# Kernel tuning notes

Measured on AMD Instinct MI355X. Metric: run time of the kernel, lower is better.

## Reference

```python
import jax, jax.numpy as jnp
import numpy as np

EMBED = 256; NH = 8; NP = 32; STRIDE = 4; FFN = 1024
NUM_IMG = 4; H = 160; W = 160; NOBJ = 2048
HD = EMBED // NH
LN_EPS = 1e-5


def setup_inputs():
    key = jax.random.key(0)
    ks = jax.random.split(key, 16)
    inp = {}
    inp["query"] = jax.random.normal(ks[0], (NOBJ, NH, 1, HD), jnp.float32)
    inp["obj_emb"] = jax.random.normal(ks[1], (NOBJ, EMBED), jnp.float32)
    inp["key_feat"] = jax.random.normal(ks[2], (NUM_IMG, EMBED, H, W), jnp.float32)
    inp["value"] = jax.random.normal(ks[3], (NUM_IMG, EMBED, H, W), jnp.float32)
    ys, xs = jnp.meshgrid(jnp.arange(H, dtype=jnp.float32), jnp.arange(W, dtype=jnp.float32), indexing="ij")
    x2d = jnp.stack([(xs + 0.5) * STRIDE, (ys + 0.5) * STRIDE], axis=0)  # (2,H,W) pixel coords
    inp["img_dense_x2d"] = jnp.broadcast_to(x2d[None], (NUM_IMG, 2, H, W)).astype(jnp.float32)
    inp["img_dense_x2d_mask"] = (jax.random.uniform(ks[4], (NUM_IMG, 1, H, W)) > 0.1).astype(jnp.float32)
    inp["obj_xy_point"] = jax.random.uniform(ks[5], (NOBJ, 2)) * jnp.array([W * STRIDE, H * STRIDE], jnp.float32)
    inp["strides"] = 2.0 ** jax.random.randint(ks[6], (NOBJ,), 2, 5).astype(jnp.float32)  # {4,8,16}
    inp["obj_img_ind"] = jax.random.randint(ks[7], (NOBJ,), 0, NUM_IMG, dtype=jnp.int32)
    s = 1.0 / np.sqrt(EMBED)
    inp["w_off"] = jax.random.uniform(ks[8], (EMBED, NH * NP * 2), minval=-s, maxval=s) * 2.5
    inp["b_off"] = jnp.zeros((NH * NP * 2,), jnp.float32)
    inp["w_out"] = jax.random.uniform(ks[9], (EMBED, EMBED), minval=-s, maxval=s)
    inp["b_out"] = jnp.zeros((EMBED,), jnp.float32)
    inp["ln1_g"] = jnp.ones((EMBED,), jnp.float32)
    inp["ln1_b"] = jnp.zeros((EMBED,), jnp.float32)
    inp["w1"] = jax.random.uniform(ks[10], (EMBED, FFN), minval=-s, maxval=s)
    inp["b1"] = jnp.zeros((FFN,), jnp.float32)
    sf = 1.0 / np.sqrt(FFN)
    inp["w2"] = jax.random.uniform(ks[11], (FFN, EMBED), minval=-sf, maxval=sf)
    inp["b2"] = jnp.zeros((EMBED,), jnp.float32)
    inp["ln2_g"] = jnp.ones((EMBED,), jnp.float32)
    inp["ln2_b"] = jnp.zeros((EMBED,), jnp.float32)
    return inp


def _unnorm(g, size):
    # align_corners=False: pixel index = ((g+1)*size - 1) / 2
    return ((g + 1.0) * size - 1.0) * 0.5


def _bilinear(gather, gx, gy, w_size, h_size, zeros_pad):
    """Bilinear sample. gather(y,x) -> (..., C). border or zeros padding."""
    ix = _unnorm(gx, w_size)
    iy = _unnorm(gy, h_size)
    x0f = jnp.floor(ix); y0f = jnp.floor(iy)
    wx1 = ix - x0f; wy1 = iy - y0f
    x0 = x0f.astype(jnp.int32); y0 = y0f.astype(jnp.int32)
    out = None
    for dx, dy, wgt in ((0, 0, (1 - wx1) * (1 - wy1)), (1, 0, wx1 * (1 - wy1)),
                        (0, 1, (1 - wx1) * wy1), (1, 1, wx1 * wy1)):
        xi = x0 + dx; yi = y0 + dy
        xc = jnp.clip(xi, 0, w_size - 1); yc = jnp.clip(yi, 0, h_size - 1)
        if zeros_pad:
            valid = (xi >= 0) & (xi < w_size) & (yi >= 0) & (yi < h_size)
            wgt = wgt * valid.astype(wgt.dtype)
        term = gather(yc, xc) * wgt[..., None]
        out = term if out is None else out + term
    return out


def _ln(x, g, b):
    m = x.mean(-1, keepdims=True)
    v = jnp.mean(jnp.square(x - m), axis=-1, keepdims=True)
    return (x - m) * jax.lax.rsqrt(v + LN_EPS) * g + b


def _forward(query, obj_emb, key_feat, value, img_dense_x2d, img_dense_x2d_mask,
             obj_xy_point, strides, obj_img_ind,
             w_off, b_off, w_out, b_out, ln1_g, ln1_b, w1, b1, w2, b2, ln2_g, ln2_b):
    N = query.shape[0]
    offsets = (obj_emb @ w_off + b_off).reshape(N, NH, NP, 2)
    loc = obj_xy_point[:, None, None] + offsets * strides[:, None, None, None]  # (N,NH,NP,2)
    gx = loc[..., 0] * (2.0 / (W * STRIDE)) - 1.0
    gy = loc[..., 1] * (2.0 / (H * STRIDE)) - 1.0
    # z grid coordinate lands exactly on slice obj_img_ind (zero depth fraction),
    # so 3D trilinear grid_sample reduces to 2D bilinear on the selected image.
    img = obj_img_ind[:, None, None]          # (N,1,1)
    head = jnp.arange(NH)[None, :, None]      # (1,NH,1)
    key_r = key_feat.reshape(NUM_IMG, NH, HD, H, W)
    val_r = value.reshape(NUM_IMG, NH, HD, H, W)
    k_s = _bilinear(lambda y, x: key_r[img, head, :, y, x], gx, gy, W, H, False)   # (N,NH,NP,HD)
    v_s = _bilinear(lambda y, x: val_r[img, head, :, y, x], gx, gy, W, H, False)   # (N,NH,NP,HD)
    x2d_s = _bilinear(lambda y, x: img_dense_x2d[img, :, y, x], gx, gy, W, H, False)       # (N,NH,NP,2)
    mask_s = _bilinear(lambda y, x: img_dense_x2d_mask[img, :, y, x], gx, gy, W, H, True)  # (N,NH,NP,1)
    q = query[:, :, 0]  # (N,NH,HD)
    a = jnp.einsum('nhd,nhpd->nhp', q, k_s) / np.sqrt(HD)
    a_sm = jax.nn.softmax(a, axis=-1) * mask_s[..., 0]
    out = jnp.einsum('nhpd,nhp->nhd', v_s, a_sm).reshape(N, EMBED)
    out = out @ w_out + b_out + obj_emb
    out = _ln(out, ln1_g, ln1_b)
    out = out + (jax.nn.relu(out @ w1 + b1) @ w2 + b2)
    out = _ln(out, ln2_g, ln2_b)
    v_samples = jnp.swapaxes(v_s, -1, -2)      # (N,NH,HD,NP)
    a_samples = a[:, :, None, :]               # (N,NH,1,NP)
    mask_samples = jnp.swapaxes(mask_s, -1, -2)  # (N,NH,1,NP)
    x2d_samples = jnp.swapaxes(x2d_s, -1, -2)    # (N,NH,2,NP)
    return (out, v_samples, a_samples, mask_samples, x2d_samples)


def reference(query, obj_emb, key_feat, value, img_dense_x2d, img_dense_x2d_mask,
              obj_xy_point, strides, obj_img_ind,
              w_off, b_off, w_out, b_out, ln1_g, ln1_b, w1, b1, w2, b2, ln2_g, ln2_b):
    return _forward(query, obj_emb, key_feat, value, img_dense_x2d, img_dense_x2d_mask,
                    obj_xy_point, strides, obj_img_ind,
                    w_off, b_off, w_out, b_out, ln1_g, ln1_b, w1, b1, w2, b2, ln2_g, ln2_b)
```

## Files before the change

kernel.cpp:

```cpp
#include <hip/hip_runtime.h>
#include <hip/hip_fp16.h>
#include <math.h>

#define NOBJ  2048
#define EMBED 256
#define NHD   8
#define NPT   32
#define HD    32
#define NUMIMG 4
#define HH    160
#define WW    160
#define FFN   1024
#define PLANE (HH*WW)
#define LN_EPS 1e-5f

typedef _Float16 f16x8 __attribute__((ext_vector_type(8)));
typedef float f32x4 __attribute__((ext_vector_type(4)));

__global__ __launch_bounds__(256) void k_offsets(
    const float* __restrict__ obj_emb, const float* __restrict__ w_off,
    const float* __restrict__ b_off, const float* __restrict__ obj_xy,
    const float* __restrict__ strides,
    float* __restrict__ cx, float* __restrict__ cy) {
  const int G = 8;
  __shared__ float s_emb[G][EMBED];
  const int t = threadIdx.x;
  const int n0 = blockIdx.x * G;
  #pragma unroll
  for (int g = 0; g < G; ++g) s_emb[g][t] = obj_emb[(n0 + g) * EMBED + t];
  __syncthreads();

  float ax[G], ay[G];
  #pragma unroll
  for (int g = 0; g < G; ++g) { ax[g] = 0.f; ay[g] = 0.f; }

  const float2* wp = (const float2*)w_off;
  for (int e = 0; e < EMBED; ++e) {
    float2 w = wp[e * 256 + t];
    #pragma unroll
    for (int g = 0; g < G; ++g) {
      float a = s_emb[g][e];
      ax[g] = fmaf(a, w.x, ax[g]);
      ay[g] = fmaf(a, w.y, ay[g]);
    }
  }
  const float bx = b_off[2 * t], by = b_off[2 * t + 1];
  #pragma unroll
  for (int g = 0; g < G; ++g) {
    const int n = n0 + g;
    const float st = strides[n];
    const float lx = obj_xy[2 * n]     + (ax[g] + bx) * st;
    const float ly = obj_xy[2 * n + 1] + (ay[g] + by) * st;
    const float gx = lx * (2.0f / (WW * 4)) - 1.0f;
    const float gy = ly * (2.0f / (HH * 4)) - 1.0f;
    const float ix = ((gx + 1.0f) * WW - 1.0f) * 0.5f;
    const float iy = ((gy + 1.0f) * HH - 1.0f) * 0.5f;
    cx[n * 256 + t] = ix;
    cy[n * 256 + t] = iy;
  }
}

__global__ __launch_bounds__(512) void k_relayout(
    const float* __restrict__ key_feat, const float* __restrict__ value,
    __half* __restrict__ kvh, int img_base) {
  __shared__ __half s[320][144];
  const int t = threadIdx.x;
  const int Y   = blockIdx.x;
  const int hp  = blockIdx.y;
  const int img = img_base + blockIdx.z;
  const int pl  = t >> 2;
  const int q   = t & 3;

  const int sub  = pl & 31;
  const int grp  = pl >> 5;
  const int head = hp * 2 + (grp >> 1);
  const int ch   = head * 32 + sub;
  const float* src = (grp & 1) ? value : key_feat;
  const float* sp  = src + ((size_t)img * 256 + ch) * PLANE
                   + (size_t)Y * 320 + q * 80;
  const int pxq = q * 80;

  #pragma unroll
  for (int i0 = 0; i0 < 20; i0 += 10) {
    float4 r[10];
    #pragma unroll
    for (int i = 0; i < 10; ++i) r[i] = *(const float4*)(sp + (i0 + i) * 4);
    #pragma unroll
    for (int i = 0; i < 10; ++i) {
      const int px = pxq + (i0 + i) * 4;
      s[px + 0][pl] = __float2half(r[i].x);
      s[px + 1][pl] = __float2half(r[i].y);
      s[px + 2][pl] = __float2half(r[i].z);
      s[px + 3][pl] = __float2half(r[i].w);
    }
  }
  __syncthreads();

  const size_t rec = (size_t)img * PLANE + (size_t)Y * 320;
  #pragma unroll
  for (int it = 0; it < 10; ++it) {
    const int flat = it * 512 + t;
    const int px = flat >> 4, j = flat & 15;
    const int4 v = *(const int4*)&s[px][j * 8];
    *(int4*)(kvh + (rec + px) * 512 + hp * 128 + j * 8) = v;
  }
}

__device__ __forceinline__ void acc8(int4 r, float w, float* acc) {
  const __half2* hp = (const __half2*)&r;
  #pragma unroll
  for (int i = 0; i < 4; ++i) {
    const float2 f = __half22float2(hp[i]);
    acc[2 * i]     = fmaf(w, f.x, acc[2 * i]);
    acc[2 * i + 1] = fmaf(w, f.y, acc[2 * i + 1]);
  }
}

__global__ __launch_bounds__(256) void k_sample_hwc(
    const float* __restrict__ query, const __half* __restrict__ kvh,
    const float* __restrict__ x2d, const float* __restrict__ x2d_mask,
    const int* __restrict__ obj_img,
    const float* __restrict__ cx, const float* __restrict__ cy,
    float* __restrict__ o_vs, float* __restrict__ o_as,
    float* __restrict__ o_ms, float* __restrict__ o_x2,
    _Float16* __restrict__ attn_h) {
  __shared__ float s_q[256];
  __shared__ float s_v[NHD * NPT * 33];
  __shared__ float s_asm[256];

  const int n = blockIdx.x;
  const int t = threadIdx.x;
  const int h = t >> 5, p = t & 31;

  s_q[t] = query[n * 256 + t];
  const int img = obj_img[n];
  const float ix = cx[n * 256 + t];
  const float iy = cy[n * 256 + t];

  const float x0f = floorf(ix), y0f = floorf(iy);
  const float wx1 = ix - x0f, wy1 = iy - y0f;
  const int x0 = (int)x0f, y0 = (int)y0f;
  const int x1 = x0 + 1, y1 = y0 + 1;
  const int x0c = min(max(x0, 0), WW - 1), x1c = min(max(x1, 0), WW - 1);
  const int y0c = min(max(y0, 0), HH - 1), y1c = min(max(y1, 0), HH - 1);
  const float w00 = (1.f - wx1) * (1.f - wy1);
  const float w10 = wx1 * (1.f - wy1);
  const float w01 = (1.f - wx1) * wy1;
  const float w11 = wx1 * wy1;
  const int o00 = y0c * WW + x0c, o10 = y0c * WW + x1c;
  const int o01 = y1c * WW + x0c, o11 = y1c * WW + x1c;

  const size_t pb = (size_t)img * PLANE;
  const int4* base = (const int4*)kvh;
  const long b0 = ((long)(pb + o00)) * 64 + h * 8;
  const long b1 = ((long)(pb + o10)) * 64 + h * 8;
  const long b2 = ((long)(pb + o01)) * 64 + h * 8;
  const long b3 = ((long)(pb + o11)) * 64 + h * 8;
  __syncthreads();

  float a_acc = 0.f;
  float* svrow = &s_v[(h * NPT + p) * 33];
  float* vout = o_vs + (size_t)(n * NHD + h) * (HD * NPT) + p;
  #pragma unroll
  for (int ch = 0; ch < 4; ++ch) {
    const int4 k0 = base[b0 + ch],     k1 = base[b1 + ch];
    const int4 k2 = base[b2 + ch],     k3 = base[b3 + ch];
    const int4 v0 = base[b0 + 4 + ch], v1 = base[b1 + 4 + ch];
    const int4 v2 = base[b2 + 4 + ch], v3 = base[b3 + 4 + ch];
    float kc[8] = {0, 0, 0, 0, 0, 0, 0, 0};
    float vc[8] = {0, 0, 0, 0, 0, 0, 0, 0};
    acc8(k0, w00, kc); acc8(k1, w10, kc); acc8(k2, w01, kc); acc8(k3, w11, kc);
    acc8(v0, w00, vc); acc8(v1, w10, vc); acc8(v2, w01, vc); acc8(v3, w11, vc);
    #pragma unroll
    for (int j = 0; j < 8; ++j) {
      const int c = ch * 8 + j;
      a_acc = fmaf(s_q[h * HD + c], kc[j], a_acc);
      svrow[c] = vc[j];
      vout[c * NPT] = vc[j];
    }
  }

  const float a = a_acc * 0.17677669529663687f;
  o_as[n * 256 + t] = a;

  const float* xb0 = x2d + (size_t)img * 2 * PLANE;
  const float* xb1 = xb0 + PLANE;
  const float x2v0 = w00 * xb0[o00] + w10 * xb0[o10] + w01 * xb0[o01] + w11 * xb0[o11];
  const float x2v1 = w00 * xb1[o00] + w10 * xb1[o10] + w01 * xb1[o01] + w11 * xb1[o11];
  o_x2[(size_t)n * 512 + h * 64 + p]      = x2v0;
  o_x2[(size_t)n * 512 + h * 64 + 32 + p] = x2v1;

  const float* mb = x2d_mask + (size_t)img * PLANE;
  const float m00 = (x0 >= 0 && x0 < WW && y0 >= 0 && y0 < HH) ? w00 : 0.f;
  const float m10 = (x1 >= 0 && x1 < WW && y0 >= 0 && y0 < HH) ? w10 : 0.f;
  const float m01 = (x0 >= 0 && x0 < WW && y1 >= 0 && y1 < HH) ? w01 : 0.f;
  const float m11 = (x1 >= 0 && x1 < WW && y1 >= 0 && y1 < HH) ? w11 : 0.f;
  const float m = m00 * mb[o00] + m10 * mb[o10] + m01 * mb[o01] + m11 * mb[o11];
  o_ms[n * 256 + t] = m;

  float mx = a;
  #pragma unroll
  for (int o = 16; o >= 1; o >>= 1) mx = fmaxf(mx, __shfl_xor(mx, o, 32));
  const float ev = expf(a - mx);
  float s = ev;
  #pragma unroll
  for (int o = 16; o >= 1; o >>= 1) s += __shfl_xor(s, o, 32);
  s_asm[t] = ev / s * m;
  __syncthreads();

  const int d = p;
  float o = 0.f;
  const float* svh = &s_v[h * NPT * 33];
  const float* amh = &s_asm[h * NPT];
  #pragma unroll
  for (int pp = 0; pp < NPT; ++pp) o = fmaf(amh[pp], svh[pp * 33 + d], o);
  attn_h[n * 256 + t] = (_Float16)o;
}

__global__ __launch_bounds__(256) void k_cvtw_all(
    const float* __restrict__ w_out, const float* __restrict__ w1,
    const float* __restrict__ w2, _Float16* __restrict__ woT,
    _Float16* __restrict__ w1T, _Float16* __restrict__ w2T) {
  __shared__ float s[32][33];
  const int id = blockIdx.x;
  const float* w; _Float16* wT; int K, N, kt, nt;
  if (id < 64)       { w = w_out; wT = woT; K = 256;  N = 256;
                       kt = id & 7;  nt = id >> 3; }
  else if (id < 320) { const int r = id - 64;  w = w1; wT = w1T;
                       K = 256;  N = 1024; kt = r & 7;  nt = r >> 3; }
  else               { const int r = id - 320; w = w2; wT = w2T;
                       K = 1024; N = 256;  kt = r & 31; nt = r >> 5; }
  const int t = threadIdx.x;
  const int k0 = kt * 32, n0 = nt * 32;
  const int nl = t & 31, kg = t >> 5;
  #pragma unroll
  for (int i = 0; i < 4; ++i) {
    const int k = kg * 4 + i;
    s[k][nl] = w[(size_t)(k0 + k) * N + n0 + nl];
  }
  __syncthreads();
  const int kl = t & 31, ng = t >> 5;
  #pragma unroll
  for (int i = 0; i < 4; ++i) {
    const int n = ng * 4 + i;
    wT[(size_t)(n0 + n) * K + k0 + kl] = (_Float16)s[kl][n];
  }
}


__global__ __launch_bounds__(256) void k_gemm_a(
    const _Float16* __restrict__ Ah, const _Float16* __restrict__ BT,
    float* __restrict__ C) {
  const int t = threadIdx.x;
  const int wv = t >> 6, lane = t & 63;
  const int r16 = lane & 15, quad = lane >> 4;
  const int m_base = blockIdx.x * 64 + wv * 16;
  const int n_base = blockIdx.y * 32;
  const _Float16* ap  = Ah + (size_t)(m_base + r16) * 256 + quad * 8;
  const _Float16* bp0 = BT + (size_t)(n_base + r16) * 256 + quad * 8;
  const _Float16* bp1 = bp0 + 16 * 256;
  f32x4 acc0 = {0.f, 0.f, 0.f, 0.f}, acc1 = {0.f, 0.f, 0.f, 0.f};
  #pragma unroll 4
  for (int kc = 0; kc < 256; kc += 32) {
    f16x8 a  = *(const f16x8*)(ap + kc);
    f16x8 b0 = *(const f16x8*)(bp0 + kc);
    f16x8 b1 = *(const f16x8*)(bp1 + kc);
    acc0 = __builtin_amdgcn_mfma_f32_16x16x32_f16(a, b0, acc0, 0, 0, 0);
    acc1 = __builtin_amdgcn_mfma_f32_16x16x32_f16(a, b1, acc1, 0, 0, 0);
  }
  float* cp = C + (size_t)(m_base + quad * 4) * 256 + n_base + r16;
  #pragma unroll
  for (int r = 0; r < 4; ++r) {
    cp[(size_t)r * 256]      = acc0[r];
    cp[(size_t)r * 256 + 16] = acc1[r];
  }
}

__global__ __launch_bounds__(256) void k_gemm_b(
    const _Float16* __restrict__ Ah, const _Float16* __restrict__ BT,
    const float* __restrict__ bias, _Float16* __restrict__ Fh) {
  const int t = threadIdx.x;
  const int wv = t >> 6, lane = t & 63;
  const int r16 = lane & 15, quad = lane >> 4;
  const int m_base = blockIdx.x * 64 + wv * 16;
  const int n_base = blockIdx.y * 32;
  const _Float16* ap  = Ah + (size_t)(m_base + r16) * 256 + quad * 8;
  const _Float16* bp0 = BT + (size_t)(n_base + r16) * 256 + quad * 8;
  const _Float16* bp1 = bp0 + 16 * 256;
  f32x4 acc0 = {0.f, 0.f, 0.f, 0.f}, acc1 = {0.f, 0.f, 0.f, 0.f};
  #pragma unroll 4
  for (int kc = 0; kc < 256; kc += 32) {
    f16x8 a  = *(const f16x8*)(ap + kc);
    f16x8 b0 = *(const f16x8*)(bp0 + kc);
    f16x8 b1 = *(const f16x8*)(bp1 + kc);
    acc0 = __builtin_amdgcn_mfma_f32_16x16x32_f16(a, b0, acc0, 0, 0, 0);
    acc1 = __builtin_amdgcn_mfma_f32_16x16x32_f16(a, b1, acc1, 0, 0, 0);
  }
  const float bb0 = bias[n_base + r16];
  const float bb1 = bias[n_base + 16 + r16];
  _Float16* fp = Fh + (size_t)(m_base + quad * 4) * 1024 + n_base + r16;
  #pragma unroll
  for (int r = 0; r < 4; ++r) {
    fp[(size_t)r * 1024]      = (_Float16)fmaxf(acc0[r] + bb0, 0.f);
    fp[(size_t)r * 1024 + 16] = (_Float16)fmaxf(acc1[r] + bb1, 0.f);
  }
}

__global__ __launch_bounds__(256) void k_gemm_c(
    const _Float16* __restrict__ Ah, const _Float16* __restrict__ BT,
    float* __restrict__ C) {
  const int t = threadIdx.x;
  const int wv = t >> 6, lane = t & 63;
  const int r16 = lane & 15, quad = lane >> 4;
  const int m_base = blockIdx.x * 64 + wv * 16;
  const int n_base = blockIdx.y * 32;
  const _Float16* ap  = Ah + (size_t)(m_base + r16) * 1024 + quad * 8;
  const _Float16* bp0 = BT + (size_t)(n_base + r16) * 1024 + quad * 8;
  const _Float16* bp1 = bp0 + 16 * 1024;
  f32x4 acc0 = {0.f, 0.f, 0.f, 0.f}, acc1 = {0.f, 0.f, 0.f, 0.f};
  #pragma unroll 4
  for (int kc = 0; kc < 1024; kc += 32) {
    f16x8 a  = *(const f16x8*)(ap + kc);
    f16x8 b0 = *(const f16x8*)(bp0 + kc);
    f16x8 b1 = *(const f16x8*)(bp1 + kc);
    acc0 = __builtin_amdgcn_mfma_f32_16x16x32_f16(a, b0, acc0, 0, 0, 0);
    acc1 = __builtin_amdgcn_mfma_f32_16x16x32_f16(a, b1, acc1, 0, 0, 0);
  }
  float* cp = C + (size_t)(m_base + quad * 4) * 256 + n_base + r16;
  #pragma unroll
  for (int r = 0; r < 4; ++r) {
    cp[(size_t)r * 256]      = acc0[r];
    cp[(size_t)r * 256 + 16] = acc1[r];
  }
}

__global__ __launch_bounds__(256) void k_ln1(
    const float* __restrict__ Y1, const float* __restrict__ b_out,
    const float* __restrict__ obj_emb, const float* __restrict__ g,
    const float* __restrict__ b, float* __restrict__ U,
    _Float16* __restrict__ Uh) {
  __shared__ float s_y[8][EMBED + 8];
  const int t = threadIdx.x;
  const int m0 = blockIdx.x * 8;
  const float bo = b_out[t];
  #pragma unroll
  for (int r = 0; r < 8; ++r)
    s_y[r][t] = Y1[(size_t)(m0 + r) * EMBED + t] + bo
                + obj_emb[(size_t)(m0 + r) * EMBED + t];
  __syncthreads();
  const int wv = t >> 6, ln = t & 63;
  #pragma unroll
  for (int k = 0; k < 2; ++k) {
    const int rr = wv * 2 + k;
    const float v0 = s_y[rr][ln], v1 = s_y[rr][ln + 64];
    const float v2 = s_y[rr][ln + 128], v3 = s_y[rr][ln + 192];
    float sum = v0 + v1 + v2 + v3;
    #pragma unroll
    for (int o = 32; o >= 1; o >>= 1) sum += __shfl_xor(sum, o);
    const float mean = sum * (1.0f / EMBED);
    const float d0 = v0 - mean, d1 = v1 - mean, d2 = v2 - mean, d3 = v3 - mean;
    float ss = d0 * d0 + d1 * d1 + d2 * d2 + d3 * d3;
    #pragma unroll
    for (int o = 32; o >= 1; o >>= 1) ss += __shfl_xor(ss, o);
    const float rstd = rsqrtf(ss * (1.0f / EMBED) + LN_EPS);
    const size_t base = (size_t)(m0 + rr) * EMBED;
    const float o0 = d0 * rstd * g[ln]       + b[ln];
    const float o1 = d1 * rstd * g[ln + 64]  + b[ln + 64];
    const float o2 = d2 * rstd * g[ln + 128] + b[ln + 128];
    const float o3 = d3 * rstd * g[ln + 192] + b[ln + 192];
    U[base + ln] = o0;         Uh[base + ln] = (_Float16)o0;
    U[base + ln + 64] = o1;    Uh[base + ln + 64] = (_Float16)o1;
    U[base + ln + 128] = o2;   Uh[base + ln + 128] = (_Float16)o2;
    U[base + ln + 192] = o3;   Uh[base + ln + 192] = (_Float16)o3;
  }
}

__global__ __launch_bounds__(256) void k_ln2(
    const float* __restrict__ Y2, const float* __restrict__ b2,
    const float* __restrict__ U, const float* __restrict__ g,
    const float* __restrict__ b, float* __restrict__ out) {
  __shared__ float s_y[8][EMBED + 8];
  const int t = threadIdx.x;
  const int m0 = blockIdx.x * 8;
  const float bb = b2[t];
  #pragma unroll
  for (int r = 0; r < 8; ++r)
    s_y[r][t] = Y2[(size_t)(m0 + r) * EMBED + t] + bb
                + U[(size_t)(m0 + r) * EMBED + t];
  __syncthreads();
  const int wv = t >> 6, ln = t & 63;
  #pragma unroll
  for (int k = 0; k < 2; ++k) {
    const int rr = wv * 2 + k;
    const float v0 = s_y[rr][ln], v1 = s_y[rr][ln + 64];
    const float v2 = s_y[rr][ln + 128], v3 = s_y[rr][ln + 192];
    float sum = v0 + v1 + v2 + v3;
    #pragma unroll
    for (int o = 32; o >= 1; o >>= 1) sum += __shfl_xor(sum, o);
    const float mean = sum * (1.0f / EMBED);
    const float d0 = v0 - mean, d1 = v1 - mean, d2 = v2 - mean, d3 = v3 - mean;
    float ss = d0 * d0 + d1 * d1 + d2 * d2 + d3 * d3;
    #pragma unroll
    for (int o = 32; o >= 1; o >>= 1) ss += __shfl_xor(ss, o);
    const float rstd = rsqrtf(ss * (1.0f / EMBED) + LN_EPS);
    const size_t base = (size_t)(m0 + rr) * EMBED;
    out[base + ln]       = d0 * rstd * g[ln]       + b[ln];
    out[base + ln + 64]  = d1 * rstd * g[ln + 64]  + b[ln + 64];
    out[base + ln + 128] = d2 * rstd * g[ln + 128] + b[ln + 128];
    out[base + ln + 192] = d3 * rstd * g[ln + 192] + b[ln + 192];
  }
}

extern "C" void kernel_launch(void* const* d_in, const int* in_sizes, int n_in,
                              void* d_out, int out_size, void* d_ws, size_t ws_size,
                              hipStream_t stream) {
  const float* query    = (const float*)d_in[0];
  const float* obj_emb  = (const float*)d_in[1];
  const float* key_feat = (const float*)d_in[2];
  const float* value    = (const float*)d_in[3];
  const float* x2d      = (const float*)d_in[4];
  const float* x2d_mask = (const float*)d_in[5];
  const float* obj_xy   = (const float*)d_in[6];
  const float* strides  = (const float*)d_in[7];
  const int*   obj_img  = (const int*)d_in[8];
  const float* w_off    = (const float*)d_in[9];
  const float* b_off    = (const float*)d_in[10];
  const float* w_out    = (const float*)d_in[11];
  const float* b_out    = (const float*)d_in[12];
  const float* ln1_g    = (const float*)d_in[13];
  const float* ln1_b    = (const float*)d_in[14];
  const float* w1       = (const float*)d_in[15];
  const float* b1       = (const float*)d_in[16];
  const float* w2       = (const float*)d_in[17];
  const float* b2       = (const float*)d_in[18];
  const float* ln2_g    = (const float*)d_in[19];
  const float* ln2_b    = (const float*)d_in[20];

  float* out = (float*)d_out;
  float* o_out = out;
  float* o_vs  = out + 524288;
  float* o_as  = out + 524288 + 16777216;
  float* o_ms  = out + 524288 + 16777216 + 524288;
  float* o_x2  = out + 524288 + 16777216 + 1048576;

  char* wsb = (char*)d_ws;
  __half*    kvh    = (__half*)wsb;
  char* B = wsb + 104857600;
  float*     cx     = (float*)(B);
  float*     Y1     = (float*)(B);
  float*     cy     = (float*)(B + 2097152);
  float*     Y2     = (float*)(B + 2097152);
  float*     U      = (float*)(B + 4194304);
  _Float16*  Fh     = (_Float16*)(B + 6291456);
  _Float16*  attn_h = (_Float16*)(B + 10485760);
  _Float16*  Uh     = (_Float16*)(B + 11534336);
  _Float16*  woT    = (_Float16*)(B + 12582912);
  _Float16*  w1T    = (_Float16*)(B + 12582912 + 131072);
  _Float16*  w2T    = (_Float16*)(B + 12582912 + 131072 + 524288);

  k_offsets<<<NOBJ / 8, 256, 0, stream>>>(obj_emb, w_off, b_off, obj_xy,
                                          strides, cx, cy);
  k_relayout<<<dim3(80, 4, 2), 512, 0, stream>>>(key_feat, value, kvh, 0);
  k_relayout<<<dim3(80, 4, 2), 512, 0, stream>>>(key_feat, value, kvh, 2);
  k_cvtw_all<<<576, 256, 0, stream>>>(w_out, w1, w2, woT, w1T, w2T);
  k_sample_hwc<<<NOBJ, 256, 0, stream>>>(query, kvh, x2d, x2d_mask, obj_img,
                                         cx, cy, o_vs, o_as, o_ms, o_x2,
                                         attn_h);
  k_gemm_a<<<dim3(32, 8), 256, 0, stream>>>(attn_h, woT, Y1);
  k_ln1<<<NOBJ / 8, 256, 0, stream>>>(Y1, b_out, obj_emb, ln1_g, ln1_b, U, Uh);
  k_gemm_b<<<dim3(32, 32), 256, 0, stream>>>(Uh, w1T, b1, Fh);
  k_gemm_c<<<dim3(32, 8), 256, 0, stream>>>(Fh, w2T, Y2);
  k_ln2<<<NOBJ / 8, 256, 0, stream>>>(Y2, b2, U, ln2_g, ln2_b, o_out);
}
```

Before: 447.4 us.

## Fuse post-attention GEMMs and layernorms into one tail kernel; merge prep kernels

Replaces the five tail kernels (out-proj GEMM, LN1, FFN up GEMM, FFN down GEMM, LN2) with a single 512-thread kernel that processes 16 rows per block and keeps intermediates in shared memory. This removes global round-trips for Y1, U, Uh, Fh and Y2, and cuts launch overhead. The offset computation and weight conversion are merged into one launch, and the sampling kernel now stages V in fp16 shared memory to shrink LDS use. Trade-offs: the tail now runs only 128 blocks, which limits parallelism, and LN variance is computed as E[x²]−mean², which is less numerically precise.

```diff
diff --git a/kernel.cpp b/kernel.cpp
--- a/kernel.cpp
+++ b/kernel.cpp
@@ -17,46 +17,71 @@
 typedef _Float16 f16x8 __attribute__((ext_vector_type(8)));
 typedef float f32x4 __attribute__((ext_vector_type(4)));
 
-__global__ __launch_bounds__(256) void k_offsets(
+__global__ __launch_bounds__(256) void k_prep(
     const float* __restrict__ obj_emb, const float* __restrict__ w_off,
     const float* __restrict__ b_off, const float* __restrict__ obj_xy,
     const float* __restrict__ strides,
-    float* __restrict__ cx, float* __restrict__ cy) {
-  const int G = 8;
-  __shared__ float s_emb[G][EMBED];
+    float* __restrict__ cx, float* __restrict__ cy,
+    const float* __restrict__ w_out, const float* __restrict__ w1,
+    const float* __restrict__ w2, _Float16* __restrict__ woT,
+    _Float16* __restrict__ w1T, _Float16* __restrict__ w2T) {
+  __shared__ float s_emb[8][EMBED];
+  __shared__ float s_t[32][33];
   const int t = threadIdx.x;
-  const int n0 = blockIdx.x * G;
-  #pragma unroll
-  for (int g = 0; g < G; ++g) s_emb[g][t] = obj_emb[(n0 + g) * EMBED + t];
-  __syncthreads();
-
-  float ax[G], ay[G];
-  #pragma unroll
-  for (int g = 0; g < G; ++g) { ax[g] = 0.f; ay[g] = 0.f; }
-
-  const float2* wp = (const float2*)w_off;
-  for (int e = 0; e < EMBED; ++e) {
-    float2 w = wp[e * 256 + t];
+  if (blockIdx.x < 256) {
+    const int G = 8;
+    const int n0 = blockIdx.x * G;
+    #pragma unroll
+    for (int g = 0; g < G; ++g) s_emb[g][t] = obj_emb[(n0 + g) * EMBED + t];
+    __syncthreads();
+    float ax[G], ay[G];
+    #pragma unroll
+    for (int g = 0; g < G; ++g) { ax[g] = 0.f; ay[g] = 0.f; }
+    const float2* wp = (const float2*)w_off;
+    for (int e = 0; e < EMBED; ++e) {
+      float2 w = wp[e * 256 + t];
+      #pragma unroll
+      for (int g = 0; g < G; ++g) {
+        float a = s_emb[g][e];
+        ax[g] = fmaf(a, w.x, ax[g]);
+        ay[g] = fmaf(a, w.y, ay[g]);
+      }
+    }
+    const float bx = b_off[2 * t], by = b_off[2 * t + 1];
     #pragma unroll
     for (int g = 0; g < G; ++g) {
-      float a = s_emb[g][e];
-      ax[g] = fmaf(a, w.x, ax[g]);
-      ay[g] = fmaf(a, w.y, ay[g]);
-    }
-  }
-  const float bx = b_off[2 * t], by = b_off[2 * t + 1];
-  #pragma unroll
-  for (int g = 0; g < G; ++g) {
-    const int n = n0 + g;
-    const float st = strides[n];
-    const float lx = obj_xy[2 * n]     + (ax[g] + bx) * st;
-    const float ly = obj_xy[2 * n + 1] + (ay[g] + by) * st;
-    const float gx = lx * (2.0f / (WW * 4)) - 1.0f;
-    const float gy = ly * (2.0f / (HH * 4)) - 1.0f;
-    const float ix = ((gx + 1.0f) * WW - 1.0f) * 0.5f;
-    const float iy = ((gy + 1.0f) * HH - 1.0f) * 0.5f;
-    cx[n * 256 + t] = ix;
-    cy[n * 256 + t] = iy;
+      const int n = n0 + g;
+      const float st = strides[n];
+      const float lx = obj_xy[2 * n]     + (ax[g] + bx) * st;
+      const float ly = obj_xy[2 * n + 1] + (ay[g] + by) * st;
+      const float gx = lx * (2.0f / (WW * 4)) - 1.0f;
+      const float gy = ly * (2.0f / (HH * 4)) - 1.0f;
+      cx[n * 256 + t] = ((gx + 1.0f) * WW - 1.0f) * 0.5f;
+      cy[n * 256 + t] = ((gy + 1.0f) * HH - 1.0f) * 0.5f;
+    }
+  } else {
+    const int id = blockIdx.x - 256;
+    const float* w; _Float16* wT; int K, N, kt, nt;
+    if (id < 64)       { w = w_out; wT = woT; K = 256;  N = 256;
+                         kt = id & 7;  nt = id >> 3; }
+    else if (id < 320) { const int r = id - 64;  w = w1; wT = w1T;
+                         K = 256;  N = 1024; kt = r & 7;  nt = r >> 3; }
+    else               { const int r = id - 320; w = w2; wT = w2T;
+                         K = 1024; N = 256;  kt = r & 31; nt = r >> 5; }
+    const int k0 = kt * 32, n0 = nt * 32;
+    const int nl = t & 31, kg = t >> 5;
+    #pragma unroll
+    for (int i = 0; i < 4; ++i) {
+      const int k = kg * 4 + i;
+      s_t[k][nl] = w[(size_t)(k0 + k) * N + n0 + nl];
+    }
+    __syncthreads();
+    const int kl = t & 31, ng = t >> 5;
+    #pragma unroll
+    for (int i = 0; i < 4; ++i) {
+      const int n = ng * 4 + i;
+      wT[(size_t)(n0 + n) * K + k0 + kl] = (_Float16)s_t[kl][n];
+    }
   }
 }
 
@@ -125,7 +150,7 @@
     float* __restrict__ o_ms, float* __restrict__ o_x2,
     _Float16* __restrict__ attn_h) {
   __shared__ float s_q[256];
-  __shared__ float s_v[NHD * NPT * 33];
+  __shared__ _Float16 s_v[NHD * NPT * 34];
   __shared__ float s_asm[256];
 
   const int n = blockIdx.x;
@@ -159,7 +184,7 @@
   __syncthreads();
 
   float a_acc = 0.f;
-  float* svrow = &s_v[(h * NPT + p) * 33];
+  _Float16* svrow = &s_v[(h * NPT + p) * 34];
   float* vout = o_vs + (size_t)(n * NHD + h) * (HD * NPT) + p;
   #pragma unroll
   for (int ch = 0; ch < 4; ++ch) {
@@ -175,7 +200,7 @@
     for (int j = 0; j < 8; ++j) {
       const int c = ch * 8 + j;
       a_acc = fmaf(s_q[h * HD + c], kc[j], a_acc);
-      svrow[c] = vc[j];
+      svrow[c] = (_Float16)vc[j];
       vout[c * NPT] = vc[j];
     }
   }
@@ -210,204 +235,159 @@
 
   const int d = p;
   float o = 0.f;
-  const float* svh = &s_v[h * NPT * 33];
+  const _Float16* svh = &s_v[h * NPT * 34];
   const float* amh = &s_asm[h * NPT];
   #pragma unroll
-  for (int pp = 0; pp < NPT; ++pp) o = fmaf(amh[pp], svh[pp * 33 + d], o);
+  for (int pp = 0; pp < NPT; ++pp)
+    o = fmaf(amh[pp], (float)svh[pp * 34 + d], o);
   attn_h[n * 256 + t] = (_Float16)o;
 }
 
-__global__ __launch_bounds__(256) void k_cvtw_all(
-    const float* __restrict__ w_out, const float* __restrict__ w1,
-    const float* __restrict__ w2, _Float16* __restrict__ woT,
-    _Float16* __restrict__ w1T, _Float16* __restrict__ w2T) {
-  __shared__ float s[32][33];
-  const int id = blockIdx.x;
-  const float* w; _Float16* wT; int K, N, kt, nt;
-  if (id < 64)       { w = w_out; wT = woT; K = 256;  N = 256;
-                       kt = id & 7;  nt = id >> 3; }
-  else if (id < 320) { const int r = id - 64;  w = w1; wT = w1T;
-                       K = 256;  N = 1024; kt = r & 7;  nt = r >> 3; }
-  else               { const int r = id - 320; w = w2; wT = w2T;
-                       K = 1024; N = 256;  kt = r & 31; nt = r >> 5; }
-  const int t = threadIdx.x;
-  const int k0 = kt * 32, n0 = nt * 32;
-  const int nl = t & 31, kg = t >> 5;
-  #pragma unroll
-  for (int i = 0; i < 4; ++i) {
-    const int k = kg * 4 + i;
-    s[k][nl] = w[(size_t)(k0 + k) * N + n0 + nl];
-  }
-  __syncthreads();
-  const int kl = t & 31, ng = t >> 5;
-  #pragma unroll
-  for (int i = 0; i < 4; ++i) {
-    const int n = ng * 4 + i;
-    wT[(size_t)(n0 + n) * K + k0 + kl] = (_Float16)s[kl][n];
-  }
-}
-
-
-__global__ __launch_bounds__(256) void k_gemm_a(
-    const _Float16* __restrict__ Ah, const _Float16* __restrict__ BT,
-    float* __restrict__ C) {
+__global__ __launch_bounds__(512) void k_tail(
+    const _Float16* __restrict__ attn_h, const _Float16* __restrict__ woT,
+    const _Float16* __restrict__ w1T, const _Float16* __restrict__ w2T,
+    const float* __restrict__ b_out, const float* __restrict__ obj_emb,
+    const float* __restrict__ g1, const float* __restrict__ bb1,
+    const float* __restrict__ b1, const float* __restrict__ b2,
+    const float* __restrict__ g2, const float* __restrict__ bb2,
+    float* __restrict__ out) {
+  __shared__ _Float16 sUh[16][264];
+  __shared__ float    sU [16][264];
+  __shared__ _Float16 sF [16][1032];
+  __shared__ float    sP[8][16];
+  __shared__ float    sQ[8][16];
   const int t = threadIdx.x;
   const int wv = t >> 6, lane = t & 63;
   const int r16 = lane & 15, quad = lane >> 4;
-  const int m_base = blockIdx.x * 64 + wv * 16;
-  const int n_base = blockIdx.y * 32;
-  const _Float16* ap  = Ah + (size_t)(m_base + r16) * 256 + quad * 8;
-  const _Float16* bp0 = BT + (size_t)(n_base + r16) * 256 + quad * 8;
-  const _Float16* bp1 = bp0 + 16 * 256;
-  f32x4 acc0 = {0.f, 0.f, 0.f, 0.f}, acc1 = {0.f, 0.f, 0.f, 0.f};
-  #pragma unroll 4
-  for (int kc = 0; kc < 256; kc += 32) {
-    f16x8 a  = *(const f16x8*)(ap + kc);
-    f16x8 b0 = *(const f16x8*)(bp0 + kc);
-    f16x8 b1 = *(const f16x8*)(bp1 + kc);
-    acc0 = __builtin_amdgcn_mfma_f32_16x16x32_f16(a, b0, acc0, 0, 0, 0);
-    acc1 = __builtin_amdgcn_mfma_f32_16x16x32_f16(a, b1, acc1, 0, 0, 0);
-  }
-  float* cp = C + (size_t)(m_base + quad * 4) * 256 + n_base + r16;
-  #pragma unroll
-  for (int r = 0; r < 4; ++r) {
-    cp[(size_t)r * 256]      = acc0[r];
-    cp[(size_t)r * 256 + 16] = acc1[r];
-  }
-}
-
-__global__ __launch_bounds__(256) void k_gemm_b(
-    const _Float16* __restrict__ Ah, const _Float16* __restrict__ BT,
-    const float* __restrict__ bias, _Float16* __restrict__ Fh) {
-  const int t = threadIdx.x;
-  const int wv = t >> 6, lane = t & 63;
-  const int r16 = lane & 15, quad = lane >> 4;
-  const int m_base = blockIdx.x * 64 + wv * 16;
-  const int n_base = blockIdx.y * 32;
-  const _Float16* ap  = Ah + (size_t)(m_base + r16) * 256 + quad * 8;
-  const _Float16* bp0 = BT + (size_t)(n_base + r16) * 256 + quad * 8;
-  const _Float16* bp1 = bp0 + 16 * 256;
-  f32x4 acc0 = {0.f, 0.f, 0.f, 0.f}, acc1 = {0.f, 0.f, 0.f, 0.f};
-  #pragma unroll 4
-  for (int kc = 0; kc < 256; kc += 32) {
-    f16x8 a  = *(const f16x8*)(ap + kc);
-    f16x8 b0 = *(const f16x8*)(bp0 + kc);
-    f16x8 b1 = *(const f16x8*)(bp1 + kc);
-    acc0 = __builtin_amdgcn_mfma_f32_16x16x32_f16(a, b0, acc0, 0, 0, 0);
-    acc1 = __builtin_amdgcn_mfma_f32_16x16x32_f16(a, b1, acc1, 0, 0, 0);
-  }
-  const float bb0 = bias[n_base + r16];
-  const float bb1 = bias[n_base + 16 + r16];
-  _Float16* fp = Fh + (size_t)(m_base + quad * 4) * 1024 + n_base + r16;
-  #pragma unroll
-  for (int r = 0; r < 4; ++r) {
-    fp[(size_t)r * 1024]      = (_Float16)fmaxf(acc0[r] + bb0, 0.f);
-    fp[(size_t)r * 1024 + 16] = (_Float16)fmaxf(acc1[r] + bb1, 0.f);
-  }
-}
-
-__global__ __launch_bounds__(256) void k_gemm_c(
-    const _Float16* __restrict__ Ah, const _Float16* __restrict__ BT,
-    float* __restrict__ C) {
-  const int t = threadIdx.x;
-  const int wv = t >> 6, lane = t & 63;
-  const int r16 = lane & 15, quad = lane >> 4;
-  const int m_base = blockIdx.x * 64 + wv * 16;
-  const int n_base = blockIdx.y * 32;
-  const _Float16* ap  = Ah + (size_t)(m_base + r16) * 1024 + quad * 8;
-  const _Float16* bp0 = BT + (size_t)(n_base + r16) * 1024 + quad * 8;
-  const _Float16* bp1 = bp0 + 16 * 1024;
-  f32x4 acc0 = {0.f, 0.f, 0.f, 0.f}, acc1 = {0.f, 0.f, 0.f, 0.f};
-  #pragma unroll 4
-  for (int kc = 0; kc < 1024; kc += 32) {
-    f16x8 a  = *(const f16x8*)(ap + kc);
-    f16x8 b0 = *(const f16x8*)(bp0 + kc);
-    f16x8 b1 = *(const f16x8*)(bp1 + kc);
-    acc0 = __builtin_amdgcn_mfma_f32_16x16x32_f16(a, b0, acc0, 0, 0, 0);
-    acc1 = __builtin_amdgcn_mfma_f32_16x16x32_f16(a, b1, acc1, 0, 0, 0);
-  }
-  float* cp = C + (size_t)(m_base + quad * 4) * 256 + n_base + r16;
-  #pragma unroll
-  for (int r = 0; r < 4; ++r) {
-    cp[(size_t)r * 256]      = acc0[r];
-    cp[(size_t)r * 256 + 16] = acc1[r];
-  }
-}
-
-__global__ __launch_bounds__(256) void k_ln1(
-    const float* __restrict__ Y1, const float* __restrict__ b_out,
-    const float* __restrict__ obj_emb, const float* __restrict__ g,
-    const float* __restrict__ b, float* __restrict__ U,
-    _Float16* __restrict__ Uh) {
-  __shared__ float s_y[8][EMBED + 8];
-  const int t = threadIdx.x;
-  const int m0 = blockIdx.x * 8;
-  const float bo = b_out[t];
-  #pragma unroll
-  for (int r = 0; r < 8; ++r)
-    s_y[r][t] = Y1[(size_t)(m0 + r) * EMBED + t] + bo
-                + obj_emb[(size_t)(m0 + r) * EMBED + t];
+  const int m0 = blockIdx.x * 16;
+
+  {
+    const int c0 = wv * 32;
+    const _Float16* ap  = attn_h + (size_t)(m0 + r16) * 256 + quad * 8;
+    const _Float16* bp0 = woT + (size_t)(c0 + r16) * 256 + quad * 8;
+    const _Float16* bp1 = bp0 + 16 * 256;
+    f32x4 acc0 = {0.f,0.f,0.f,0.f}, acc1 = {0.f,0.f,0.f,0.f};
+    #pragma unroll
+    for (int kc = 0; kc < 256; kc += 32) {
+      f16x8 a  = *(const f16x8*)(ap + kc);
+      f16x8 b0 = *(const f16x8*)(bp0 + kc);
+      f16x8 b1f = *(const f16x8*)(bp1 + kc);
+      acc0 = __builtin_amdgcn_mfma_f32_16x16x32_f16(a, b0, acc0, 0, 0, 0);
+      acc1 = __builtin_amdgcn_mfma_f32_16x16x32_f16(a, b1f, acc1, 0, 0, 0);
+    }
+    const int col0 = c0 + r16, col1 = c0 + 16 + r16;
+    const float bo0 = b_out[col0], bo1 = b_out[col1];
+    float v0[4], v1[4];
+    #pragma unroll
+    for (int r = 0; r < 4; ++r) {
+      const size_t row = (size_t)(m0 + quad * 4 + r) * 256;
+      v0[r] = acc0[r] + bo0 + obj_emb[row + col0];
+      v1[r] = acc1[r] + bo1 + obj_emb[row + col1];
+    }
+    #pragma unroll
+    for (int r = 0; r < 4; ++r) {
+      float s = v0[r] + v1[r];
+      float q = v0[r] * v0[r] + v1[r] * v1[r];
+      #pragma unroll
+      for (int m = 1; m < 16; m <<= 1) {
+        s += __shfl_xor(s, m);
+        q += __shfl_xor(q, m);
+      }
+      if (r16 == 0) { sP[wv][quad * 4 + r] = s; sQ[wv][quad * 4 + r] = q; }
+    }
+    __syncthreads();
+    const float g0 = g1[col0], be0 = bb1[col0];
+    const float g1v = g1[col1], be1 = bb1[col1];
+    #pragma unroll
+    for (int r = 0; r < 4; ++r) {
+      const int rr = quad * 4 + r;
+      float S = 0.f, Q = 0.f;
+      #pragma unroll
+      for (int w = 0; w < 8; ++w) { S += sP[w][rr]; Q += sQ[w][rr]; }
+      const float mean = S * (1.0f / EMBED);
+      const float var  = Q * (1.0f / EMBED) - mean * mean;
+      const float rstd = rsqrtf(var + LN_EPS);
+      const float u0 = (v0[r] - mean) * rstd * g0 + be0;
+      const float u1 = (v1[r] - mean) * rstd * g1v + be1;
+      sU[rr][col0] = u0;  sUh[rr][col0] = (_Float16)u0;
+      sU[rr][col1] = u1;  sUh[rr][col1] = (_Float16)u1;
+    }
+  }
   __syncthreads();
-  const int wv = t >> 6, ln = t & 63;
-  #pragma unroll
-  for (int k = 0; k < 2; ++k) {
-    const int rr = wv * 2 + k;
-    const float v0 = s_y[rr][ln], v1 = s_y[rr][ln + 64];
-    const float v2 = s_y[rr][ln + 128], v3 = s_y[rr][ln + 192];
-    float sum = v0 + v1 + v2 + v3;
-    #pragma unroll
-    for (int o = 32; o >= 1; o >>= 1) sum += __shfl_xor(sum, o);
-    const float mean = sum * (1.0f / EMBED);
-    const float d0 = v0 - mean, d1 = v1 - mean, d2 = v2 - mean, d3 = v3 - mean;
-    float ss = d0 * d0 + d1 * d1 + d2 * d2 + d3 * d3;
-    #pragma unroll
-    for (int o = 32; o >= 1; o >>= 1) ss += __shfl_xor(ss, o);
-    const float rstd = rsqrtf(ss * (1.0f / EMBED) + LN_EPS);
-    const size_t base = (size_t)(m0 + rr) * EMBED;
-    const float o0 = d0 * rstd * g[ln]       + b[ln];
-    const float o1 = d1 * rstd * g[ln + 64]  + b[ln + 64];
-    const float o2 = d2 * rstd * g[ln + 128] + b[ln + 128];
-    const float o3 = d3 * rstd * g[ln + 192] + b[ln + 192];
-    U[base + ln] = o0;         Uh[base + ln] = (_Float16)o0;
-    U[base + ln + 64] = o1;    Uh[base + ln + 64] = (_Float16)o1;
-    U[base + ln + 128] = o2;   Uh[base + ln + 128] = (_Float16)o2;
-    U[base + ln + 192] = o3;   Uh[base + ln + 192] = (_Float16)o3;
-  }
-}
-
-__global__ __launch_bounds__(256) void k_ln2(
-    const float* __restrict__ Y2, const float* __restrict__ b2,
-    const float* __restrict__ U, const float* __restrict__ g,
-    const float* __restrict__ b, float* __restrict__ out) {
-  __shared__ float s_y[8][EMBED + 8];
-  const int t = threadIdx.x;
-  const int m0 = blockIdx.x * 8;
-  const float bb = b2[t];
-  #pragma unroll
-  for (int r = 0; r < 8; ++r)
-    s_y[r][t] = Y2[(size_t)(m0 + r) * EMBED + t] + bb
-                + U[(size_t)(m0 + r) * EMBED + t];
+
+  {
+    const int c0 = wv * 128;
+    f32x4 acc[8];
+    #pragma unroll
+    for (int i = 0; i < 8; ++i) acc[i] = (f32x4){0.f,0.f,0.f,0.f};
+    for (int kc = 0; kc < 256; kc += 32) {
+      f16x8 a = *(const f16x8*)&sUh[r16][quad * 8 + kc];
+      #pragma unroll
+      for (int nt = 0; nt < 8; ++nt) {
+        f16x8 b = *(const f16x8*)(w1T + (size_t)(c0 + nt * 16 + r16) * 256
+                                  + quad * 8 + kc);
+        acc[nt] = __builtin_amdgcn_mfma_f32_16x16x32_f16(a, b, acc[nt], 0, 0, 0);
+      }
+    }
+    #pragma unroll
+    for (int nt = 0; nt < 8; ++nt) {
+      const int col = c0 + nt * 16 + r16;
+      const float bb = b1[col];
+      #pragma unroll
+      for (int r = 0; r < 4; ++r)
+        sF[quad * 4 + r][col] = (_Float16)fmaxf(acc[nt][r] + bb, 0.f);
+    }
+  }
   __syncthreads();
-  const int wv = t >> 6, ln = t & 63;
-  #pragma unroll
-  for (int k = 0; k < 2; ++k) {
-    const int rr = wv * 2 + k;
-    const float v0 = s_y[rr][ln], v1 = s_y[rr][ln + 64];
-    const float v2 = s_y[rr][ln + 128], v3 = s_y[rr][ln + 192];
-    float sum = v0 + v1 + v2 + v3;
-    #pragma unroll
-    for (int o = 32; o >= 1; o >>= 1) sum += __shfl_xor(sum, o);
-    const float mean = sum * (1.0f / EMBED);
-    const float d0 = v0 - mean, d1 = v1 - mean, d2 = v2 - mean, d3 = v3 - mean;
-    float ss = d0 * d0 + d1 * d1 + d2 * d2 + d3 * d3;
-    #pragma unroll
-    for (int o = 32; o >= 1; o >>= 1) ss += __shfl_xor(ss, o);
-    const float rstd = rsqrtf(ss * (1.0f / EMBED) + LN_EPS);
-    const size_t base = (size_t)(m0 + rr) * EMBED;
-    out[base + ln]       = d0 * rstd * g[ln]       + b[ln];
-    out[base + ln + 64]  = d1 * rstd * g[ln + 64]  + b[ln + 64];
-    out[base + ln + 128] = d2 * rstd * g[ln + 128] + b[ln + 128];
-    out[base + ln + 192] = d3 * rstd * g[ln + 192] + b[ln + 192];
+
+  {
+    const int c0 = wv * 32;
+    const _Float16* bp0 = w2T + (size_t)(c0 + r16) * 1024 + quad * 8;
+    const _Float16* bp1 = bp0 + 16 * 1024;
+    f32x4 acc0 = {0.f,0.f,0.f,0.f}, acc1 = {0.f,0.f,0.f,0.f};
+    for (int kc = 0; kc < 1024; kc += 32) {
+      f16x8 a  = *(const f16x8*)&sF[r16][quad * 8 + kc];
+      f16x8 b0 = *(const f16x8*)(bp0 + kc);
+      f16x8 b1f = *(const f16x8*)(bp1 + kc);
+      acc0 = __builtin_amdgcn_mfma_f32_16x16x32_f16(a, b0, acc0, 0, 0, 0);
+      acc1 = __builtin_amdgcn_mfma_f32_16x16x32_f16(a, b1f, acc1, 0, 0, 0);
+    }
+    const int col0 = c0 + r16, col1 = c0 + 16 + r16;
+    const float bo0 = b2[col0], bo1 = b2[col1];
+    float v0[4], v1[4];
+    #pragma unroll
+    for (int r = 0; r < 4; ++r) {
+      const int rr = quad * 4 + r;
+      v0[r] = acc0[r] + bo0 + sU[rr][col0];
+      v1[r] = acc1[r] + bo1 + sU[rr][col1];
+    }
+    #pragma unroll
+    for (int r = 0; r < 4; ++r) {
+      float s = v0[r] + v1[r];
+      float q = v0[r] * v0[r] + v1[r] * v1[r];
+      #pragma unroll
+      for (int m = 1; m < 16; m <<= 1) {
+        s += __shfl_xor(s, m);
+        q += __shfl_xor(q, m);
+      }
+      if (r16 == 0) { sP[wv][quad * 4 + r] = s; sQ[wv][quad * 4 + r] = q; }
+    }
+    __syncthreads();
+    const float g0 = g2[col0], be0 = bb2[col0];
+    const float g1v = g2[col1], be1 = bb2[col1];
+    #pragma unroll
+    for (int r = 0; r < 4; ++r) {
+      const int rr = quad * 4 + r;
+      float S = 0.f, Q = 0.f;
+      #pragma unroll
+      for (int w = 0; w < 8; ++w) { S += sP[w][rr]; Q += sQ[w][rr]; }
+      const float mean = S * (1.0f / EMBED);
+      const float var  = Q * (1.0f / EMBED) - mean * mean;
+      const float rstd = rsqrtf(var + LN_EPS);
+      const size_t row = (size_t)(m0 + rr) * 256;
+      out[row + col0] = (v0[r] - mean) * rstd * g0 + be0;
+      out[row + col1] = (v1[r] - mean) * rstd * g1v + be1;
+    }
   }
 }
 
@@ -447,28 +427,20 @@
   __half*    kvh    = (__half*)wsb;
   char* B = wsb + 104857600;
   float*     cx     = (float*)(B);
-  float*     Y1     = (float*)(B);
   float*     cy     = (float*)(B + 2097152);
-  float*     Y2     = (float*)(B + 2097152);
-  float*     U      = (float*)(B + 4194304);
-  _Float16*  Fh     = (_Float16*)(B + 6291456);
-  _Float16*  attn_h = (_Float16*)(B + 10485760);
-  _Float16*  Uh     = (_Float16*)(B + 11534336);
-  _Float16*  woT    = (_Float16*)(B + 12582912);
-  _Float16*  w1T    = (_Float16*)(B + 12582912 + 131072);
-  _Float16*  w2T    = (_Float16*)(B + 12582912 + 131072 + 524288);
-
-  k_offsets<<<NOBJ / 8, 256, 0, stream>>>(obj_emb, w_off, b_off, obj_xy,
-                                          strides, cx, cy);
+  _Float16*  attn_h = (_Float16*)(B + 4194304);
+  _Float16*  woT    = (_Float16*)(B + 5242880);
+  _Float16*  w1T    = (_Float16*)(B + 5242880 + 131072);
+  _Float16*  w2T    = (_Float16*)(B + 5242880 + 131072 + 524288);
+
+  k_prep<<<832, 256, 0, stream>>>(obj_emb, w_off, b_off, obj_xy, strides,
+                                  cx, cy, w_out, w1, w2, woT, w1T, w2T);
   k_relayout<<<dim3(80, 4, 2), 512, 0, stream>>>(key_feat, value, kvh, 0);
   k_relayout<<<dim3(80, 4, 2), 512, 0, stream>>>(key_feat, value, kvh, 2);
-  k_cvtw_all<<<576, 256, 0, stream>>>(w_out, w1, w2, woT, w1T, w2T);
   k_sample_hwc<<<NOBJ, 256, 0, stream>>>(query, kvh, x2d, x2d_mask, obj_img,
                                          cx, cy, o_vs, o_as, o_ms, o_x2,
                                          attn_h);
-  k_gemm_a<<<dim3(32, 8), 256, 0, stream>>>(attn_h, woT, Y1);
-  k_ln1<<<NOBJ / 8, 256, 0, stream>>>(Y1, b_out, obj_emb, ln1_g, ln1_b, U, Uh);
-  k_gemm_b<<<dim3(32, 32), 256, 0, stream>>>(Uh, w1T, b1, Fh);
-  k_gemm_c<<<dim3(32, 8), 256, 0, stream>>>(Fh, w2T, Y2);
-  k_ln2<<<NOBJ / 8, 256, 0, stream>>>(Y2, b2, U, ln2_g, ln2_b, o_out);
-}
+  k_tail<<<NOBJ / 16, 512, 0, stream>>>(attn_h, woT, w1T, w2T, b_out, obj_emb,
+                                        ln1_g, ln1_b, b1, b2, ln2_g, ln2_b,
+                                        o_out);
+}
```

Result: slower. 487.1 us (+8.9%).
